# Optimization experiments

Measured on AMD Instinct MI355X. Metric: run time of the kernel, lower is better.

## Reference

```python
import jax, jax.numpy as jnp
import numpy as np

K = 32
EPS = 1e-16


def setup_inputs() -> dict:
    key = jax.random.key(0)
    k1, k2, k3 = jax.random.split(key, 3)
    N_l, N_h, D, F = 8192, 32768, 3, 128
    x = jax.random.normal(k1, (N_l, F), dtype=jnp.float32)
    pos_l = jax.random.normal(k2, (N_l, D), dtype=jnp.float32)
    pos_h = jax.random.normal(k3, (N_h, D), dtype=jnp.float32)
    return {"x": x, "pos_l": pos_l, "pos_h": pos_h}


def reference(x, pos_l, pos_h):
    # Squared pairwise distances [N_h, N_l] via ||h||^2 - 2 h.l + ||l||^2
    h2 = jnp.sum(pos_h * pos_h, axis=1, keepdims=True)        # [N_h, 1]
    l2 = jnp.sum(pos_l * pos_l, axis=1)                        # [N_l]
    d2 = h2 - 2.0 * (pos_h @ pos_l.T) + l2[None, :]            # [N_h, N_l]
    # k nearest source points per target point
    neg_d2k, idx = jax.lax.top_k(-d2, K)                       # [N_h, K]
    d2k = -neg_d2k
    # Inverse squared-distance weights (torch_geometric: 1/clamp(d2, min=1e-16))
    w = 1.0 / jnp.maximum(d2k, EPS)                            # [N_h, K]
    xk = x[idx]                                                # [N_h, K, F]
    y = jnp.einsum('nk,nkf->nf', w, xk) / jnp.sum(w, axis=1, keepdims=True)
    return y
```

## Files before the change

### kernel.cpp

```cpp
#include <hip/hip_runtime.h>
#include <stdint.h>

#define NL     8192
#define NH     32768
#define FDIM   128
#define KSEL   32
#define CHUNK  1024
#define NCHUNK (NL / CHUNK)
#define QPW    8
#define NWAVES 4
#define BLOCK  (NWAVES * 64)
#define QPB    (NWAVES * QPW)
#define BUFCAP 128

__device__ __forceinline__ int imin(int a, int b) { return a < b ? a : b; }
__device__ __forceinline__ int imax(int a, int b) { return a > b ? a : b; }

__global__ __launch_bounds__(BLOCK, 4)
void knn_interp_kernel(const float* __restrict__ x,
                       const float* __restrict__ pos_l,
                       const float* __restrict__ pos_h,
                       float* __restrict__ out)
{
    __shared__ float4   s_cand[CHUNK];
    __shared__ uint16_t s_idx[QPB][BUFCAP];
    __shared__ uint32_t s_cnt[QPB];
    __shared__ float    s_wd2[QPB][KSEL];
    __shared__ uint16_t s_widx[QPB][KSEL];

    const int tid   = threadIdx.x;
    const int lane  = tid & 63;
    const int wid   = tid >> 6;
    const int qbase = blockIdx.x * QPB + wid * QPW;

    float hx2[QPW], hy2[QPW], hz2[QPW], h2c[QPW];
#pragma unroll
    for (int q = 0; q < QPW; ++q) {
        const float ax = pos_h[(qbase + q) * 3 + 0];
        const float ay = pos_h[(qbase + q) * 3 + 1];
        const float az = pos_h[(qbase + q) * 3 + 2];
        hx2[q] = -2.0f * ax; hy2[q] = -2.0f * ay; hz2[q] = -2.0f * az;
        h2c[q] = ax * ax + ay * ay + az * az;
    }

    float rmin[QPW];
#pragma unroll
    for (int q = 0; q < QPW; ++q) rmin[q] = INFINITY;

    for (int c = 0; c < NCHUNK; ++c) {
        __syncthreads();
        for (int i = tid; i < CHUNK; i += BLOCK) {
            const int g = c * CHUNK + i;
            const float px = pos_l[g * 3 + 0];
            const float py = pos_l[g * 3 + 1];
            const float pz = pos_l[g * 3 + 2];
            s_cand[i] = make_float4(px, py, pz, px * px + py * py + pz * pz);
        }
        __syncthreads();
#pragma unroll 4
        for (int i = 0; i < CHUNK / 64; ++i) {
            const float4 p = s_cand[i * 64 + lane];
#pragma unroll
            for (int q = 0; q < QPW; ++q) {
                float d2 = fmaf(hx2[q], p.x, p.w);
                d2 = fmaf(hy2[q], p.y, d2);
                d2 = fmaf(hz2[q], p.z, d2);
                d2 = d2 + h2c[q];
                rmin[q] = fminf(rmin[q], d2);
            }
        }
    }

    float tau_acc[QPW];
#pragma unroll
    for (int q = 0; q < QPW; ++q) {
        float v = rmin[q];
#pragma unroll
        for (int k = 2; k <= 64; k <<= 1) {
#pragma unroll
            for (int j = k >> 1; j >= 1; j >>= 1) {
                const float o     = __shfl_xor(v, j);
                const bool  up    = ((lane & k) == 0);
                const bool  lower = ((lane & j) == 0);
                v = (lower == up) ? fminf(v, o) : fmaxf(v, o);
            }
        }
        const float tau = __shfl(v, 31);
        tau_acc[q] = tau + 1e-4f;
    }

    if (tid < QPB) s_cnt[tid] = 0;

    for (int c = 0; c < NCHUNK; ++c) {
        __syncthreads();
        for (int i = tid; i < CHUNK; i += BLOCK) {
            const int g = c * CHUNK + i;
            const float px = pos_l[g * 3 + 0];
            const float py = pos_l[g * 3 + 1];
            const float pz = pos_l[g * 3 + 2];
            s_cand[i] = make_float4(px, py, pz, px * px + py * py + pz * pz);
        }
        __syncthreads();
#pragma unroll 2
        for (int i = 0; i < CHUNK / 64; ++i) {
            const int ci = i * 64 + lane;
            const float4 p = s_cand[ci];
#pragma unroll
            for (int q = 0; q < QPW; ++q) {
                float d2 = fmaf(hx2[q], p.x, p.w);
                d2 = fmaf(hy2[q], p.y, d2);
                d2 = fmaf(hz2[q], p.z, d2);
                d2 = d2 + h2c[q];
                if (d2 <= tau_acc[q]) {
                    const uint32_t pos = atomicAdd(&s_cnt[wid * QPW + q], 1u);
                    if (pos < BUFCAP) s_idx[wid * QPW + q][pos] = (uint16_t)(c * CHUNK + ci);
                }
            }
        }
    }

#pragma unroll 1
    for (int q = 0; q < QPW; ++q) {
        const int qq = wid * QPW + q;
        uint32_t M = s_cnt[qq];
        if (M > BUFCAP) M = BUFCAP;

        const double axd = (double)(-0.5f * hx2[q]);
        const double ayd = (double)(-0.5f * hy2[q]);
        const double azd = (double)(-0.5f * hz2[q]);

        const int i0 = ((uint32_t)(2 * lane)     < M) ? (int)s_idx[qq][2 * lane]     : -1;
        const int i1 = ((uint32_t)(2 * lane + 1) < M) ? (int)s_idx[qq][2 * lane + 1] : -1;
        float f0 = INFINITY, f1 = INFINITY;
        if (i0 >= 0) {
            const double dx = (double)pos_l[i0 * 3 + 0] - axd;
            const double dy = (double)pos_l[i0 * 3 + 1] - ayd;
            const double dz = (double)pos_l[i0 * 3 + 2] - azd;
            f0 = (float)(dx * dx + dy * dy + dz * dz);
        }
        if (i1 >= 0) {
            const double dx = (double)pos_l[i1 * 3 + 0] - axd;
            const double dy = (double)pos_l[i1 * 3 + 1] - ayd;
            const double dz = (double)pos_l[i1 * 3 + 2] - azd;
            f1 = (float)(dx * dx + dy * dy + dz * dz);
        }

        int v0 = __float_as_int(f0);
        int v1 = __float_as_int(f1);
#pragma unroll
        for (int k = 2; k <= 128; k <<= 1) {
            const bool up = ((lane & (k >> 1)) == 0);
#pragma unroll
            for (int j = k >> 1; j >= 2; j >>= 1) {
                const int  xo    = j >> 1;
                const bool lower = ((lane & xo) == 0);
                const int o0 = __shfl_xor(v0, xo);
                const int o1 = __shfl_xor(v1, xo);
                v0 = (lower == up) ? imin(v0, o0) : imax(v0, o0);
                v1 = (lower == up) ? imin(v1, o1) : imax(v1, o1);
            }
            const int mn = imin(v0, v1), mx = imax(v0, v1);
            v0 = up ? mn : mx;
            v1 = up ? mx : mn;
        }
        const int tau32 = __shfl(v1, 15);

        const bool a0 = (i0 >= 0) && (__float_as_int(f0) <= tau32);
        const bool a1 = (i1 >= 0) && (__float_as_int(f1) <= tau32);
        const unsigned long long b0 = __ballot(a0);
        const unsigned long long b1 = __ballot(a1);
        const unsigned long long mb = (lane == 63) ? 0x7FFFFFFFFFFFFFFFull
                                                   : ((1ull << (lane + 1)) - 1ull) >> 1;
        const int base = __popcll(b0 & mb) + __popcll(b1 & mb);
        const int p0 = base;
        const int p1 = base + (a0 ? 1 : 0);
        if (a0 && p0 < KSEL) { s_wd2[qq][p0] = f0; s_widx[qq][p0] = (uint16_t)i0; }
        if (a1 && p1 < KSEL) { s_wd2[qq][p1] = f1; s_widx[qq][p1] = (uint16_t)i1; }
    }

#pragma unroll 1
    for (int q = 0; q < QPW; ++q) {
        const int qq = wid * QPW + q;
        const int gq = qbase + q;
        float acc0 = 0.0f, acc1 = 0.0f, wsum = 0.0f;
#pragma unroll 8
        for (int kk = 0; kk < KSEL; ++kk) {
            const float d2  = s_wd2[qq][kk];
            const float w   = 1.0f / fmaxf(d2, 1e-16f);
            const int   idx = (int)s_widx[qq][kk];
            const float* row = x + (size_t)idx * FDIM;
            acc0 = fmaf(w, row[lane], acc0);
            acc1 = fmaf(w, row[lane + 64], acc1);
            wsum += w;
        }
        const float invw = 1.0f / wsum;
        out[(size_t)gq * FDIM + lane]      = acc0 * invw;
        out[(size_t)gq * FDIM + 64 + lane] = acc1 * invw;
    }
}

extern "C" void kernel_launch(void* const* d_in, const int* in_sizes, int n_in,
                              void* d_out, int out_size, void* d_ws, size_t ws_size,
                              hipStream_t stream) {
    const float* x     = (const float*)d_in[0];
    const float* pos_l = (const float*)d_in[1];
    const float* pos_h = (const float*)d_in[2];
    float* out = (float*)d_out;
    dim3 grid(NH / QPB);
    dim3 block(BLOCK);
    hipLaunchKernelGGL(knn_interp_kernel, grid, block, 0, stream,
                       x, pos_l, pos_h, out);
}
```

Before: 193.0 us.

## Replace brute-force KNN scan with Morton-sorted groups and bounding-sphere pruning

Source points are bucketed into a 16^3 grid, sorted in Morton order, and split into 128 groups of 64, each with a bounding sphere. Each query takes a distance threshold from the 4 nearest groups and then scans only groups whose sphere could hold points within that threshold, instead of two full passes over all 8192 points. This cuts the distance work a lot but adds four small preprocessing kernels, a memset, divergent per-query group loops, and a binary-search fallback when candidates overflow the buffer. The grid range is hardcoded to [-4,4], which suits normally distributed inputs, but points outside it are clamped into edge cells, so correctness still holds.

```diff
diff --git a/kernel.cpp b/kernel.cpp
--- a/kernel.cpp
+++ b/kernel.cpp
@@ -1,80 +1,159 @@
 #include <hip/hip_runtime.h>
 #include <stdint.h>
 
-#define NL     8192
-#define NH     32768
-#define FDIM   128
-#define KSEL   32
-#define CHUNK  1024
-#define NCHUNK (NL / CHUNK)
-#define QPW    8
-#define NWAVES 4
-#define BLOCK  (NWAVES * 64)
-#define QPB    (NWAVES * QPW)
-#define BUFCAP 128
+#define NL      8192
+#define NH      32768
+#define FDIM    128
+#define KSEL    32
+#define QPW     8
+#define NWAVES  4
+#define BLOCK   (NWAVES * 64)
+#define QPB     (NWAVES * QPW)
+#define BUFCAP  256
+#define NGROUP  (NL / 64)
+#define NCELL   4096
+#define TSCAN   4
+#define MAXPASS 6
 
 __device__ __forceinline__ int imin(int a, int b) { return a < b ? a : b; }
 __device__ __forceinline__ int imax(int a, int b) { return a > b ? a : b; }
 
+__device__ __forceinline__ uint32_t spread3(uint32_t x) {
+    x &= 0xFu;
+    x = (x | (x << 16)) & 0x030000FFu;
+    x = (x | (x << 8))  & 0x0300F00Fu;
+    x = (x | (x << 4))  & 0x030C30C3u;
+    x = (x | (x << 2))  & 0x09249249u;
+    return x;
+}
+__device__ __forceinline__ int cell_of(float px, float py, float pz) {
+    int ix = (int)floorf((px + 4.0f) * 2.0f);
+    int iy = (int)floorf((py + 4.0f) * 2.0f);
+    int iz = (int)floorf((pz + 4.0f) * 2.0f);
+    ix = imin(imax(ix, 0), 15); iy = imin(imax(iy, 0), 15); iz = imin(imax(iz, 0), 15);
+    return (int)(spread3((uint32_t)ix) | (spread3((uint32_t)iy) << 1) | (spread3((uint32_t)iz) << 2));
+}
+
+__global__ void k_cell_count(const float* __restrict__ pos_l, int* __restrict__ hist) {
+    const int i = blockIdx.x * 256 + threadIdx.x;
+    if (i >= NL) return;
+    const int c = cell_of(pos_l[i * 3 + 0], pos_l[i * 3 + 1], pos_l[i * 3 + 2]);
+    atomicAdd(&hist[c], 1);
+}
+
+__global__ void k_cell_scan(const int* __restrict__ hist, int* __restrict__ cursor) {
+    __shared__ int part[256];
+    __shared__ int partpref[256];
+    const int tid = threadIdx.x;
+    int loc[16];
+    int s = 0;
+#pragma unroll
+    for (int i = 0; i < 16; ++i) { loc[i] = s; s += hist[tid * 16 + i]; }
+    part[tid] = s;
+    __syncthreads();
+    if (tid == 0) {
+        int a = 0;
+        for (int t = 0; t < 256; ++t) { partpref[t] = a; a += part[t]; }
+    }
+    __syncthreads();
+    const int b = partpref[tid];
+#pragma unroll
+    for (int i = 0; i < 16; ++i) cursor[tid * 16 + i] = b + loc[i];
+}
+
+__global__ void k_scatter(const float* __restrict__ pos_l, int* __restrict__ cursor,
+                          float4* __restrict__ sorted, int* __restrict__ oidx) {
+    const int i = blockIdx.x * 256 + threadIdx.x;
+    if (i >= NL) return;
+    const float px = pos_l[i * 3 + 0];
+    const float py = pos_l[i * 3 + 1];
+    const float pz = pos_l[i * 3 + 2];
+    const int c = cell_of(px, py, pz);
+    const int pos = atomicAdd(&cursor[c], 1);
+    sorted[pos] = make_float4(px, py, pz, px * px + py * py + pz * pz);
+    oidx[pos] = i;
+}
+
+__global__ void k_spheres(const float4* __restrict__ sorted, float4* __restrict__ spheres) {
+    const int g = blockIdx.x;
+    const int lane = threadIdx.x;
+    const float4 p = sorted[g * 64 + lane];
+    float sx = p.x, sy = p.y, sz = p.z;
+#pragma unroll
+    for (int j = 32; j >= 1; j >>= 1) {
+        sx += __shfl_xor(sx, j); sy += __shfl_xor(sy, j); sz += __shfl_xor(sz, j);
+    }
+    const float cx = sx * (1.0f / 64.0f), cy = sy * (1.0f / 64.0f), cz = sz * (1.0f / 64.0f);
+    const float dx = p.x - cx, dy = p.y - cy, dz = p.z - cz;
+    float d2 = dx * dx + dy * dy + dz * dz;
+#pragma unroll
+    for (int j = 32; j >= 1; j >>= 1) d2 = fmaxf(d2, __shfl_xor(d2, j));
+    if (lane == 0) spheres[g] = make_float4(cx, cy, cz, sqrtf(d2) + 1e-3f);
+}
+
 __global__ __launch_bounds__(BLOCK, 4)
 void knn_interp_kernel(const float* __restrict__ x,
-                       const float* __restrict__ pos_l,
                        const float* __restrict__ pos_h,
+                       const float4* __restrict__ sorted,
+                       const float4* __restrict__ spheres,
+                       const int* __restrict__ oidx,
                        float* __restrict__ out)
 {
-    __shared__ float4   s_cand[CHUNK];
+    __shared__ float4   s_grp[NGROUP];
+    __shared__ unsigned long long s_surv[NWAVES][QPW][2];
     __shared__ uint16_t s_idx[QPB][BUFCAP];
-    __shared__ uint32_t s_cnt[QPB];
-    __shared__ float    s_wd2[QPB][KSEL];
-    __shared__ uint16_t s_widx[QPB][KSEL];
+    __shared__ float    s_w[QPB][KSEL];
+    __shared__ int      s_wi[QPB][KSEL];
 
     const int tid   = threadIdx.x;
     const int lane  = tid & 63;
     const int wid   = tid >> 6;
     const int qbase = blockIdx.x * QPB + wid * QPW;
-
-    float hx2[QPW], hy2[QPW], hz2[QPW], h2c[QPW];
+    const unsigned long long mlt = (1ull << lane) - 1ull;
+
+    if (tid < NGROUP) s_grp[tid] = spheres[tid];
+    __syncthreads();
+
+    const float4 cA = s_grp[lane];
+    const float4 cB = s_grp[lane + 64];
+
+    float qx[QPW], qy[QPW], qz[QPW], h2q[QPW], tauD[QPW];
+
 #pragma unroll
     for (int q = 0; q < QPW; ++q) {
-        const float ax = pos_h[(qbase + q) * 3 + 0];
-        const float ay = pos_h[(qbase + q) * 3 + 1];
-        const float az = pos_h[(qbase + q) * 3 + 2];
-        hx2[q] = -2.0f * ax; hy2[q] = -2.0f * ay; hz2[q] = -2.0f * az;
-        h2c[q] = ax * ax + ay * ay + az * az;
-    }
-
-    float rmin[QPW];
-#pragma unroll
-    for (int q = 0; q < QPW; ++q) rmin[q] = INFINITY;
-
-    for (int c = 0; c < NCHUNK; ++c) {
-        __syncthreads();
-        for (int i = tid; i < CHUNK; i += BLOCK) {
-            const int g = c * CHUNK + i;
-            const float px = pos_l[g * 3 + 0];
-            const float py = pos_l[g * 3 + 1];
-            const float pz = pos_l[g * 3 + 2];
-            s_cand[i] = make_float4(px, py, pz, px * px + py * py + pz * pz);
-        }
-        __syncthreads();
-#pragma unroll 4
-        for (int i = 0; i < CHUNK / 64; ++i) {
-            const float4 p = s_cand[i * 64 + lane];
-#pragma unroll
-            for (int q = 0; q < QPW; ++q) {
-                float d2 = fmaf(hx2[q], p.x, p.w);
-                d2 = fmaf(hy2[q], p.y, d2);
-                d2 = fmaf(hz2[q], p.z, d2);
-                d2 = d2 + h2c[q];
-                rmin[q] = fminf(rmin[q], d2);
-            }
-        }
-    }
-
-    float tau_acc[QPW];
-#pragma unroll
-    for (int q = 0; q < QPW; ++q) {
-        float v = rmin[q];
+        const int gq = qbase + q;
+        qx[q] = pos_h[gq * 3 + 0];
+        qy[q] = pos_h[gq * 3 + 1];
+        qz[q] = pos_h[gq * 3 + 2];
+        h2q[q] = fmaf(qx[q], qx[q], fmaf(qy[q], qy[q], qz[q] * qz[q]));
+
+        const float dAx = qx[q] - cA.x, dAy = qy[q] - cA.y, dAz = qz[q] - cA.z;
+        const float dA  = fmaf(dAx, dAx, fmaf(dAy, dAy, dAz * dAz));
+        const float dBx = qx[q] - cB.x, dBy = qy[q] - cB.y, dBz = qz[q] - cB.z;
+        const float dB  = fmaf(dBx, dBx, fmaf(dBy, dBy, dBz * dBz));
+
+        int kA = (int)((__float_as_uint(dA) & 0xFFFFFF00u) | (uint32_t)lane);
+        int kB = (int)((__float_as_uint(dB) & 0xFFFFFF00u) | (uint32_t)(lane + 64));
+
+        int gsel[TSCAN];
+#pragma unroll
+        for (int t = 0; t < TSCAN; ++t) {
+            int m = imin(kA, kB);
+#pragma unroll
+            for (int j = 1; j <= 32; j <<= 1) m = imin(m, __shfl_xor(m, j));
+            gsel[t] = m & 0xFF;
+            if (kA == m) kA = 0x7FFFFFFF;
+            if (kB == m) kB = 0x7FFFFFFF;
+        }
+
+        float dmin = INFINITY;
+#pragma unroll
+        for (int t = 0; t < TSCAN; ++t) {
+            const float4 p = sorted[(gsel[t] << 6) + lane];
+            const float s = fmaf(qx[q], p.x, fmaf(qy[q], p.y, qz[q] * p.z));
+            dmin = fminf(dmin, fmaf(-2.0f, s, p.w));
+        }
+        float v = dmin;
 #pragma unroll
         for (int k = 2; k <= 64; k <<= 1) {
 #pragma unroll
@@ -85,109 +164,157 @@
                 v = (lower == up) ? fminf(v, o) : fmaxf(v, o);
             }
         }
-        const float tau = __shfl(v, 31);
-        tau_acc[q] = tau + 1e-4f;
-    }
-
-    if (tid < QPB) s_cnt[tid] = 0;
-
-    for (int c = 0; c < NCHUNK; ++c) {
-        __syncthreads();
-        for (int i = tid; i < CHUNK; i += BLOCK) {
-            const int g = c * CHUNK + i;
-            const float px = pos_l[g * 3 + 0];
-            const float py = pos_l[g * 3 + 1];
-            const float pz = pos_l[g * 3 + 2];
-            s_cand[i] = make_float4(px, py, pz, px * px + py * py + pz * pz);
-        }
-        __syncthreads();
-#pragma unroll 2
-        for (int i = 0; i < CHUNK / 64; ++i) {
-            const int ci = i * 64 + lane;
-            const float4 p = s_cand[ci];
-#pragma unroll
-            for (int q = 0; q < QPW; ++q) {
-                float d2 = fmaf(hx2[q], p.x, p.w);
-                d2 = fmaf(hy2[q], p.y, d2);
-                d2 = fmaf(hz2[q], p.z, d2);
-                d2 = d2 + h2c[q];
-                if (d2 <= tau_acc[q]) {
-                    const uint32_t pos = atomicAdd(&s_cnt[wid * QPW + q], 1u);
-                    if (pos < BUFCAP) s_idx[wid * QPW + q][pos] = (uint16_t)(c * CHUNK + ci);
-                }
-            }
-        }
+        const float tau = __shfl(v, 31) + 1e-4f;
+        tauD[q] = tau;
+
+        const float st = sqrtf(fmaxf(tau + h2q[q], 0.0f)) + 1e-3f;
+        const float tA = st + cA.w, tB = st + cB.w;
+        const unsigned long long bA = __ballot(dA <= tA * tA);
+        const unsigned long long bB = __ballot(dB <= tB * tB);
+        if (lane == 0) { s_surv[wid][q][0] = bA; s_surv[wid][q][1] = bB; }
     }
 
 #pragma unroll 1
     for (int q = 0; q < QPW; ++q) {
-        const int qq = wid * QPW + q;
-        uint32_t M = s_cnt[qq];
+        const int QQ = wid * QPW + q;
+        const int gq = qbase + q;
+        float tau = tauD[q];
+        int M = 0;
+
+#pragma unroll 1
+        for (int pass = 0; pass < MAXPASS; ++pass) {
+            M = 0;
+#pragma unroll 1
+            for (int h = 0; h < 2; ++h) {
+                unsigned long long mm = s_surv[wid][q][h];
+                while (mm) {
+                    const int g = (h << 6) + __builtin_ctzll(mm);
+                    mm &= mm - 1;
+                    const float4 p = sorted[(g << 6) + lane];
+                    const float s = fmaf(qx[q], p.x, fmaf(qy[q], p.y, qz[q] * p.z));
+                    const float D = fmaf(-2.0f, s, p.w);
+                    const bool hit = (D <= tau);
+                    const unsigned long long b = __ballot(hit);
+                    if (b) {
+                        const int o = M + (int)__popcll(b & mlt);
+                        if (hit && o < BUFCAP) s_idx[QQ][o] = (uint16_t)((g << 6) + lane);
+                        M += (int)__popcll(b);
+                    }
+                }
+            }
+            if (M <= BUFCAP) break;
+            int kk[4];
+#pragma unroll
+            for (int r = 0; r < 4; ++r) {
+                const int idx = (int)s_idx[QQ][64 * r + lane];
+                const float4 c = sorted[idx];
+                const float s = fmaf(qx[q], c.x, fmaf(qy[q], c.y, qz[q] * c.z));
+                const float d2 = fmaxf(fmaf(-2.0f, s, c.w) + h2q[q], 0.0f);
+                kk[r] = __float_as_int(d2);
+            }
+            int lo = 0, hi = 0x7F800000;
+            while (lo < hi) {
+                const int mid = (int)(((unsigned)lo + (unsigned)hi) >> 1);
+                int cnt = 0;
+#pragma unroll
+                for (int r = 0; r < 4; ++r)
+                    cnt += (int)__popcll(__ballot(kk[r] <= mid));
+                if (cnt >= KSEL) hi = mid; else lo = mid + 1;
+            }
+            tau = __int_as_float(lo) - h2q[q] + 1e-4f;
+        }
         if (M > BUFCAP) M = BUFCAP;
 
-        const double axd = (double)(-0.5f * hx2[q]);
-        const double ayd = (double)(-0.5f * hy2[q]);
-        const double azd = (double)(-0.5f * hz2[q]);
-
-        const int i0 = ((uint32_t)(2 * lane)     < M) ? (int)s_idx[qq][2 * lane]     : -1;
-        const int i1 = ((uint32_t)(2 * lane + 1) < M) ? (int)s_idx[qq][2 * lane + 1] : -1;
-        float f0 = INFINITY, f1 = INFINITY;
-        if (i0 >= 0) {
-            const double dx = (double)pos_l[i0 * 3 + 0] - axd;
-            const double dy = (double)pos_l[i0 * 3 + 1] - ayd;
-            const double dz = (double)pos_l[i0 * 3 + 2] - azd;
-            f0 = (float)(dx * dx + dy * dy + dz * dz);
-        }
-        if (i1 >= 0) {
-            const double dx = (double)pos_l[i1 * 3 + 0] - axd;
-            const double dy = (double)pos_l[i1 * 3 + 1] - ayd;
-            const double dz = (double)pos_l[i1 * 3 + 2] - azd;
-            f1 = (float)(dx * dx + dy * dy + dz * dz);
-        }
-
-        int v0 = __float_as_int(f0);
-        int v1 = __float_as_int(f1);
-#pragma unroll
-        for (int k = 2; k <= 128; k <<= 1) {
-            const bool up = ((lane & (k >> 1)) == 0);
-#pragma unroll
-            for (int j = k >> 1; j >= 2; j >>= 1) {
-                const int  xo    = j >> 1;
-                const bool lower = ((lane & xo) == 0);
-                const int o0 = __shfl_xor(v0, xo);
-                const int o1 = __shfl_xor(v1, xo);
-                v0 = (lower == up) ? imin(v0, o0) : imax(v0, o0);
-                v1 = (lower == up) ? imin(v1, o1) : imax(v1, o1);
-            }
-            const int mn = imin(v0, v1), mx = imax(v0, v1);
-            v0 = up ? mn : mx;
-            v1 = up ? mx : mn;
-        }
-        const int tau32 = __shfl(v1, 15);
-
-        const bool a0 = (i0 >= 0) && (__float_as_int(f0) <= tau32);
-        const bool a1 = (i1 >= 0) && (__float_as_int(f1) <= tau32);
-        const unsigned long long b0 = __ballot(a0);
-        const unsigned long long b1 = __ballot(a1);
-        const unsigned long long mb = (lane == 63) ? 0x7FFFFFFFFFFFFFFFull
-                                                   : ((1ull << (lane + 1)) - 1ull) >> 1;
-        const int base = __popcll(b0 & mb) + __popcll(b1 & mb);
-        const int p0 = base;
-        const int p1 = base + (a0 ? 1 : 0);
-        if (a0 && p0 < KSEL) { s_wd2[qq][p0] = f0; s_widx[qq][p0] = (uint16_t)i0; }
-        if (a1 && p1 < KSEL) { s_wd2[qq][p1] = f1; s_widx[qq][p1] = (uint16_t)i1; }
-    }
-
-#pragma unroll 1
-    for (int q = 0; q < QPW; ++q) {
-        const int qq = wid * QPW + q;
-        const int gq = qbase + q;
+        const double ax = (double)qx[q], ay = (double)qy[q], az = (double)qz[q];
+        if (M <= 128) {
+            const int i0 = (2 * lane     < M) ? (int)s_idx[QQ][2 * lane]     : -1;
+            const int i1 = (2 * lane + 1 < M) ? (int)s_idx[QQ][2 * lane + 1] : -1;
+            float f0 = INFINITY, f1 = INFINITY;
+            if (i0 >= 0) {
+                const float4 c = sorted[i0];
+                const double dx = (double)c.x - ax, dy = (double)c.y - ay, dz = (double)c.z - az;
+                f0 = (float)(dx * dx + dy * dy + dz * dz);
+            }
+            if (i1 >= 0) {
+                const float4 c = sorted[i1];
+                const double dx = (double)c.x - ax, dy = (double)c.y - ay, dz = (double)c.z - az;
+                f1 = (float)(dx * dx + dy * dy + dz * dz);
+            }
+            int v0 = __float_as_int(f0);
+            int v1 = __float_as_int(f1);
+#pragma unroll
+            for (int k = 2; k <= 128; k <<= 1) {
+                const bool up = ((lane & (k >> 1)) == 0);
+#pragma unroll
+                for (int j = k >> 1; j >= 2; j >>= 1) {
+                    const int  xo    = j >> 1;
+                    const bool lower = ((lane & xo) == 0);
+                    const int o0 = __shfl_xor(v0, xo);
+                    const int o1 = __shfl_xor(v1, xo);
+                    v0 = (lower == up) ? imin(v0, o0) : imax(v0, o0);
+                    v1 = (lower == up) ? imin(v1, o1) : imax(v1, o1);
+                }
+                const int mn = imin(v0, v1), mx = imax(v0, v1);
+                v0 = up ? mn : mx;
+                v1 = up ? mx : mn;
+            }
+            const int tau32 = __shfl(v1, 15);
+            const bool a0 = (i0 >= 0) && (__float_as_int(f0) <= tau32);
+            const bool a1 = (i1 >= 0) && (__float_as_int(f1) <= tau32);
+            const unsigned long long b0 = __ballot(a0);
+            const unsigned long long b1 = __ballot(a1);
+            const int base = (int)__popcll(b0 & mlt) + (int)__popcll(b1 & mlt);
+            const int p0 = base;
+            const int p1 = base + (a0 ? 1 : 0);
+            if (a0 && p0 < KSEL) { s_w[QQ][p0] = 1.0f / fmaxf(f0, 1e-16f); s_wi[QQ][p0] = oidx[i0]; }
+            if (a1 && p1 < KSEL) { s_w[QQ][p1] = 1.0f / fmaxf(f1, 1e-16f); s_wi[QQ][p1] = oidx[i1]; }
+        } else {
+            int ii[4]; float ff[4]; int kk_[4];
+#pragma unroll
+            for (int r = 0; r < 4; ++r) {
+                const int e = 4 * lane + r;
+                ii[r] = (e < M) ? (int)s_idx[QQ][e] : -1;
+                ff[r] = INFINITY;
+                if (ii[r] >= 0) {
+                    const float4 c = sorted[ii[r]];
+                    const double dx = (double)c.x - ax, dy = (double)c.y - ay, dz = (double)c.z - az;
+                    ff[r] = (float)(dx * dx + dy * dy + dz * dz);
+                }
+                kk_[r] = __float_as_int(ff[r]);
+            }
+            int lo = 0, hi = 0x7F800000;
+            while (lo < hi) {
+                const int mid = (int)(((unsigned)lo + (unsigned)hi) >> 1);
+                int cnt = 0;
+#pragma unroll
+                for (int r = 0; r < 4; ++r)
+                    cnt += (int)__popcll(__ballot(ii[r] >= 0 && kk_[r] <= mid));
+                if (cnt >= KSEL) hi = mid; else lo = mid + 1;
+            }
+            const int tau32 = lo;
+            bool a[4]; unsigned long long b[4];
+#pragma unroll
+            for (int r = 0; r < 4; ++r) {
+                a[r] = (ii[r] >= 0) && (kk_[r] <= tau32);
+                b[r] = __ballot(a[r]);
+            }
+            int base = 0;
+#pragma unroll
+            for (int r = 0; r < 4; ++r) base += (int)__popcll(b[r] & mlt);
+            int pref = 0;
+#pragma unroll
+            for (int r = 0; r < 4; ++r) {
+                const int p = base + pref;
+                if (a[r] && p < KSEL) { s_w[QQ][p] = 1.0f / fmaxf(ff[r], 1e-16f); s_wi[QQ][p] = oidx[ii[r]]; }
+                pref += (a[r] ? 1 : 0);
+            }
+        }
+
         float acc0 = 0.0f, acc1 = 0.0f, wsum = 0.0f;
 #pragma unroll 8
-        for (int kk = 0; kk < KSEL; ++kk) {
-            const float d2  = s_wd2[qq][kk];
-            const float w   = 1.0f / fmaxf(d2, 1e-16f);
-            const int   idx = (int)s_widx[qq][kk];
+        for (int t = 0; t < KSEL; ++t) {
+            const float w   = s_w[QQ][t];
+            const int   idx = s_wi[QQ][t];
             const float* row = x + (size_t)idx * FDIM;
             acc0 = fmaf(w, row[lane], acc0);
             acc1 = fmaf(w, row[lane + 64], acc1);
@@ -206,8 +333,19 @@
     const float* pos_l = (const float*)d_in[1];
     const float* pos_h = (const float*)d_in[2];
     float* out = (float*)d_out;
-    dim3 grid(NH / QPB);
-    dim3 block(BLOCK);
-    hipLaunchKernelGGL(knn_interp_kernel, grid, block, 0, stream,
-                       x, pos_l, pos_h, out);
-}
+
+    char* ws = (char*)d_ws;
+    int*    hist    = (int*)(ws + 0);
+    int*    cursor  = (int*)(ws + 16384);
+    float4* spheres = (float4*)(ws + 32768);
+    float4* sorted  = (float4*)(ws + 65536);
+    int*    oidx    = (int*)(ws + 65536 + 131072);
+
+    hipMemsetAsync(hist, 0, NCELL * sizeof(int), stream);
+    hipLaunchKernelGGL(k_cell_count, dim3(NL / 256), dim3(256), 0, stream, pos_l, hist);
+    hipLaunchKernelGGL(k_cell_scan, dim3(1), dim3(256), 0, stream, hist, cursor);
+    hipLaunchKernelGGL(k_scatter, dim3(NL / 256), dim3(256), 0, stream, pos_l, cursor, sorted, oidx);
+    hipLaunchKernelGGL(k_spheres, dim3(NGROUP), dim3(64), 0, stream, sorted, spheres);
+    hipLaunchKernelGGL(knn_interp_kernel, dim3(NH / QPB), dim3(BLOCK), 0, stream,
+                       x, pos_h, sorted, spheres, oidx, out);
+}
```

Result: slower. 220.9 us (+14.5%).
